# Kernel optimization log

Hardware: AMD Instinct MI355X
Metric: run time of the kernel (lower is better)

## Reference

```python
import math
import jax, jax.numpy as jnp
import numpy as np

B, T, E = 2, 2048, 2048
H, HKV = 16, 4
DH = E // H              # 128
ROT_DIM = DH             # rotary_pct = 1.0 -> 128
ROT_HALF = ROT_DIM // 2  # RotaryEmbedding is built with dim=ROT_DIM//2=64; only these dims rotate
MAX_SEQ = 2048


def _rope_tables():
    # theta = 10000 ** (-arange(0, dim, 2)/dim) with dim = ROT_HALF
    theta = 10000.0 ** (-jnp.arange(0, ROT_HALF, 2, dtype=jnp.float32) / ROT_HALF)  # [ROT_HALF//2]
    pos = jnp.arange(MAX_SEQ, dtype=jnp.float32)
    angles = pos[:, None] * theta[None, :]   # [MAX_SEQ, ROT_HALF//2]
    return jnp.cos(angles), jnp.sin(angles)


def _apply_rotary(q, k, start_pos):
    # q: [B,T,H,ROT_DIM], k: [B,T,HKV,ROT_DIM]; rotate only first ROT_HALF dims (interleaved pairs)
    cos, sin = _rope_tables()
    t = q.shape[1]
    cos = jax.lax.dynamic_slice_in_dim(cos, start_pos, t, axis=0)[None, :, None, :]
    sin = jax.lax.dynamic_slice_in_dim(sin, start_pos, t, axis=0)[None, :, None, :]

    def rot(a):
        a_rot, a_pass = a[..., :ROT_HALF], a[..., ROT_HALF:]
        x, y = a_rot[..., 0::2], a_rot[..., 1::2]
        rx = x * cos - y * sin
        ry = x * sin + y * cos
        rotated = jnp.stack([rx, ry], axis=-1).reshape(*a_rot.shape)
        return jnp.concatenate([rotated, a_pass], axis=-1)

    return rot(q), rot(k)


def setup_inputs() -> dict:
    key = jax.random.key(0)
    ks = jax.random.split(key, 9)
    s = 0.02  # weight scale for sane logits
    return {
        "x": jax.random.normal(ks[0], (B, T, E), dtype=jnp.float32),
        "Wq": jax.random.normal(ks[1], (E, H * DH), dtype=jnp.float32) * s,
        "bq": jax.random.normal(ks[2], (H * DH,), dtype=jnp.float32) * s,
        "Wk": jax.random.normal(ks[3], (E, HKV * DH), dtype=jnp.float32) * s,
        "bk": jax.random.normal(ks[4], (HKV * DH,), dtype=jnp.float32) * s,
        "Wv": jax.random.normal(ks[5], (E, HKV * DH), dtype=jnp.float32) * s,
        "bv": jax.random.normal(ks[6], (HKV * DH,), dtype=jnp.float32) * s,
        "Wo": jax.random.normal(ks[7], (E, E), dtype=jnp.float32) * s,
        "bo": jax.random.normal(ks[8], (E,), dtype=jnp.float32) * s,
        "start_pos": 0,
    }


def reference(x, Wq, bq, Wk, bk, Wv, bv, Wo, bo, start_pos):
    b, t, _ = x.shape
    q = (x @ Wq + bq).reshape(b, t, H, DH)
    k = (x @ Wk + bk).reshape(b, t, HKV, DH)
    v = (x @ Wv + bv).reshape(b, t, HKV, DH)

    q, k = _apply_rotary(q, k, start_pos)

    group = H // HKV
    k = jnp.repeat(k, group, axis=2)  # [b,t,H,DH]
    v = jnp.repeat(v, group, axis=2)

    # scores: [b,H,t,t]
    scores = jnp.einsum("bqhd,bkhd->bhqk", q, k) / math.sqrt(DH)
    causal = jnp.tril(jnp.ones((t, t), dtype=bool))
    scores = jnp.where(causal[None, None], scores, -jnp.inf)
    probs = jax.nn.softmax(scores, axis=-1)

    out = jnp.einsum("bhqk,bkhd->bqhd", probs, v).reshape(b, t, H * DH)
    return out @ Wo + bo
```

## Files before the change

kernel.cpp:

```cpp
#include <hip/hip_runtime.h>

typedef __attribute__((ext_vector_type(8))) short short8;
typedef __attribute__((ext_vector_type(4))) float f32x4;
typedef __attribute__((ext_vector_type(16))) float f32x16;

#define DEVFN __device__ __forceinline__

DEVFN unsigned short f2bf(float f) {
  unsigned int u = __builtin_bit_cast(unsigned int, f);
  u += 0x7FFFu + ((u >> 16) & 1u);
  return (unsigned short)(u >> 16);
}
DEVFN float bf2f(unsigned int u) { return __builtin_bit_cast(float, u << 16); }

DEVFN unsigned int cvtpk_bf16(float lo, float hi) {
  unsigned int d;
  asm("v_cvt_pk_bf16_f32 %0, %1, %2" : "=v"(d) : "v"(lo), "v"(hi));
  return d;
}
DEVFN void plswap32(unsigned int& a, unsigned int& b) {
  asm("v_permlane32_swap_b32 %0, %1" : "+v"(a), "+v"(b));
}
DEVFN float bcast32(float v, int srclane) {
  int r = __builtin_amdgcn_ds_bpermute(srclane * 4, __builtin_bit_cast(int, v));
  return __builtin_bit_cast(float, r);
}

__global__ __launch_bounds__(256) void prep_all(
    const float* __restrict__ Wq, const float* __restrict__ Wk, const float* __restrict__ Wv,
    const float* __restrict__ Wo, const float* __restrict__ bq, const float* __restrict__ bk,
    const float* __restrict__ bv, const float* __restrict__ x,
    unsigned short* __restrict__ Wqkvt, unsigned short* __restrict__ Wot,
    unsigned short* __restrict__ xb, float* __restrict__ cost, float* __restrict__ sint,
    float* __restrict__ bcat) {
  __shared__ float lds[32][33];
  const int bid = blockIdx.x, tid = threadIdx.x;
  if (bid < 10240) {
    const float* W; unsigned short* Wt; int ncols, bx, by;
    if (bid < 4096)      { W = Wq; Wt = Wqkvt;                        ncols = 2048; bx = bid & 63; by = bid >> 6; }
    else if (bid < 5120) { int l = bid - 4096; W = Wk; Wt = Wqkvt + (size_t)2048 * 2048; ncols = 512; bx = l & 15; by = l >> 4; }
    else if (bid < 6144) { int l = bid - 5120; W = Wv; Wt = Wqkvt + (size_t)2560 * 2048; ncols = 512; bx = l & 15; by = l >> 4; }
    else                 { int l = bid - 6144; W = Wo; Wt = Wot;      ncols = 2048; bx = l & 63; by = l >> 6; }
    int n0 = bx * 32, k0 = by * 32;
    int tx = tid & 31, ty = tid >> 5;
    #pragma unroll
    for (int i = 0; i < 4; i++) {
      int kr = ty + i * 8;
      lds[kr][tx] = W[(size_t)(k0 + kr) * ncols + n0 + tx];
    }
    __syncthreads();
    #pragma unroll
    for (int i = 0; i < 4; i++) {
      int nr = ty + i * 8;
      Wt[(size_t)(n0 + nr) * 2048 + k0 + tx] = f2bf(lds[tx][nr]);
    }
  } else if (bid < 14336) {
    int gid = (bid - 10240) * 256 + tid;
    const float4* xv = (const float4*)x;
    float4 a = xv[(size_t)gid * 2], b = xv[(size_t)gid * 2 + 1];
    short8 u;
    u[0] = (short)f2bf(a.x); u[1] = (short)f2bf(a.y); u[2] = (short)f2bf(a.z); u[3] = (short)f2bf(a.w);
    u[4] = (short)f2bf(b.x); u[5] = (short)f2bf(b.y); u[6] = (short)f2bf(b.z); u[7] = (short)f2bf(b.w);
    *(short8*)(xb + (size_t)gid * 8) = u;
  } else if (bid < 14592) {
    int gid = (bid - 14336) * 256 + tid;
    int pos = gid >> 5, i = gid & 31;
    float theta = powf(10000.0f, -(float)(2 * i) / 64.0f);
    float ang = (float)pos * theta;
    cost[gid] = cosf(ang);
    sint[gid] = sinf(ang);
  } else {
    int i = (bid - 14592) * 256 + tid;
    float v;
    if (i < 2048) v = bq[i];
    else if (i < 2560) v = bk[i - 2048];
    else v = bv[i - 2560];
    bcat[i] = v;
  }
}

__global__ __launch_bounds__(256) void scatter_all(
    const unsigned short* __restrict__ QKVb, const float* __restrict__ cost,
    const float* __restrict__ sint, const int* __restrict__ spp,
    unsigned short* __restrict__ QFr, unsigned short* __restrict__ KFr,
    unsigned short* __restrict__ VFr) {
  __shared__ __align__(16) unsigned short lds[64 * 128];
  const int bid = blockIdx.x, tid = threadIdx.x;
  if (bid < 20480) {
    int NH, LOG2NH, colOff, gid;
    unsigned short* dst;
    float scale;
    if (bid < 16384) { NH = 16; LOG2NH = 4; colOff = 0;    dst = QFr; scale = 0.12751743f; gid = bid * 256 + tid; }
    else             { NH = 4;  LOG2NH = 2; colOff = 2048; dst = KFr; scale = 1.0f;        gid = (bid - 16384) * 256 + tid; }
    int j = gid & 63;
    int h = (gid >> 6) & (NH - 1);
    int m = gid >> (6 + LOG2NH);
    int t = m & 2047;
    int b = m >> 11;
    const unsigned short* src = QKVb + (size_t)m * 3072 + colOff + h * 128 + 2 * j;
    unsigned int pair = *(const unsigned int*)src;
    float xv = bf2f(pair & 0xFFFFu), yv = bf2f(pair >> 16);
    float rx, ry;
    if (j < 32) {
      int pos = (spp[0] + t) & 2047;
      float c = cost[pos * 32 + j], s = sint[pos * 32 + j];
      rx = xv * c - yv * s;
      ry = xv * s + yv * c;
    } else { rx = xv; ry = yv; }
    rx *= scale; ry *= scale;
    int d0 = 2 * j;
    size_t off = (size_t)(b * NH + h) * 262144 + (t >> 5) * 4096 + (d0 >> 4) * 512
               + ((d0 >> 3) & 1) * 256 + (t & 31) * 8 + (d0 & 7);
    unsigned int outp = (unsigned int)f2bf(rx) | ((unsigned int)f2bf(ry) << 16);
    *(unsigned int*)(dst + off) = outp;
  } else {
    int l = bid - 20480;
    int t0 = (l & 31) * 64;
    int bk = l >> 5;
    const unsigned short* src = QKVb + (size_t)(bk >> 2) * 2048 * 3072 + 2560 + (bk & 3) * 128;
    #pragma unroll
    for (int c = 0; c < 4; c++) {
      int idx = c * 256 + tid;
      int tr = idx >> 4, dc = idx & 15;
      short8 v = *(const short8*)(src + (size_t)(t0 + tr) * 3072 + dc * 8);
      *(short8*)((char*)lds + tr * 256 + 16 * (dc ^ (tr >> 3))) = v;
    }
    __syncthreads();
    unsigned short* dstb = VFr + (size_t)bk * 262144;
    #pragma unroll
    for (int c2 = 0; c2 < 4; c2++) {
      int idx2 = c2 * 256 + tid;
      int tc = idx2 & 7, d = idx2 >> 3;
      short8 u;
      #pragma unroll
      for (int e = 0; e < 8; e++) {
        int t = 8 * tc + e;
        u[e] = *(const short*)((char*)lds + t * 256 + 16 * ((d >> 3) ^ tc) + (d & 7) * 2);
      }
      size_t off = (size_t)(t0 >> 6) * 8192 + ((d >> 5) * 4 + ((tc >> 1) & 3)) * 512
                 + (tc & 1) * 256 + (d & 31) * 8;
      *(short8*)(dstb + off) = u;
    }
  }
}

template<bool BF16OUT>
__global__ __launch_bounds__(512, 1) void gemm256(
    const unsigned short* __restrict__ A, const unsigned short* __restrict__ Bt,
    const float* __restrict__ bias, void* __restrict__ Cout, int M, int N, int K, int NTX) {
  __shared__ __align__(16) unsigned short lds[3][24576];
  const int tid = threadIdx.x;
  const int lane = tid & 63, w = tid >> 6;
  const int wr = w >> 1, wc = w & 1;
  const int f = blockIdx.x;
  const int cpx = gridDim.x >> 3;
  const int fs = (f & 7) * cpx + (f >> 3);
  const int m0 = (fs / NTX) * 256, n0 = (fs % NTX) * 128;
  const int NT = K >> 6;

  f32x4 acc[4][4];
  #pragma unroll
  for (int i = 0; i < 4; i++)
    #pragma unroll
    for (int j = 0; j < 4; j++)
      #pragma unroll
      for (int r = 0; r < 4; r++) acc[i][j][r] = 0.f;

  const int r8 = tid >> 3;
  const int c8 = (tid & 7) ^ (r8 & 7);
  const unsigned short* Asrc = A  + (size_t)(m0 + r8) * K + c8 * 8;
  const unsigned short* Bsrc = Bt + (size_t)(n0 + r8) * K + c8 * 8;
  const int woff = w * 512;

  auto STAGE = [&](int t) {
    unsigned short* bb = &lds[t % 3][0];
    const unsigned short* as = Asrc + t * 64;
    const unsigned short* bs = Bsrc + t * 64;
    #pragma unroll
    for (int l = 0; l < 2; l++) {
      __builtin_amdgcn_global_load_lds(
        (const __attribute__((address_space(1))) unsigned int*)(as + (size_t)l * 64 * K),
        (__attribute__((address_space(3))) unsigned int*)(bb + l * 4096 + woff), 16, 0, 0);
      __builtin_amdgcn_global_load_lds(
        (const __attribute__((address_space(1))) unsigned int*)(as + (size_t)(128 + l * 64) * K),
        (__attribute__((address_space(3))) unsigned int*)(bb + 8192 + l * 4096 + woff), 16, 0, 0);
      __builtin_amdgcn_global_load_lds(
        (const __attribute__((address_space(1))) unsigned int*)(bs + (size_t)l * 64 * K),
        (__attribute__((address_space(3))) unsigned int*)(bb + 16384 + l * 4096 + woff), 16, 0, 0);
    }
  };

  STAGE(0);
  STAGE(1);

  const int lr = lane & 15;
  const int q4 = lane >> 4;
  const int p7 = lane & 7;
  const int so0 = ((q4 ^ p7) * 8);
  const int so1 = (((q4 ^ 4) ^ p7) * 8);
  const int aBase = ((wr & 2) ? 8192 : 0) + ((wr & 1) * 64 + lr) * 64;
  const int bBase = 16384 + (wc * 64 + lr) * 64;

  for (int t = 0; t < NT; t++) {
    if (t + 1 < NT) asm volatile("s_waitcnt vmcnt(6)" ::: "memory");
    else            asm volatile("s_waitcnt vmcnt(0)" ::: "memory");
    __builtin_amdgcn_sched_barrier(0);
    __builtin_amdgcn_s_barrier();
    __builtin_amdgcn_sched_barrier(0);
    if (t + 2 < NT) STAGE(t + 2);
    const unsigned short* bb = &lds[t % 3][0];
    #pragma unroll
    for (int ks = 0; ks < 2; ks++) {
      const int so = ks ? so1 : so0;
      short8 af[4], bfr[4];
      #pragma unroll
      for (int mi = 0; mi < 4; mi++)
        af[mi] = *(const short8*)(bb + aBase + mi * 1024 + so);
      #pragma unroll
      for (int ni = 0; ni < 4; ni++)
        bfr[ni] = *(const short8*)(bb + bBase + ni * 1024 + so);
      __builtin_amdgcn_s_setprio(1);
      #pragma unroll
      for (int mi = 0; mi < 4; mi++)
        #pragma unroll
        for (int ni = 0; ni < 4; ni++)
          acc[mi][ni] = __builtin_amdgcn_mfma_f32_16x16x32_bf16(af[mi], bfr[ni], acc[mi][ni], 0, 0, 0);
      __builtin_amdgcn_s_setprio(0);
    }
  }

  const int cl = lane & 15, rq = lane >> 4;
  #pragma unroll
  for (int mi = 0; mi < 4; mi++) {
    #pragma unroll
    for (int ni = 0; ni < 4; ni++) {
      int gn = n0 + wc * 64 + ni * 16 + cl;
      float bv = bias[gn];
      #pragma unroll
      for (int r = 0; r < 4; r++) {
        int gm = m0 + wr * 64 + mi * 16 + rq * 4 + r;
        float v = acc[mi][ni][r] + bv;
        if (BF16OUT) ((unsigned short*)Cout)[(size_t)gm * N + gn] = f2bf(v);
        else ((float*)Cout)[(size_t)gm * N + gn] = v;
      }
    }
  }
}

__global__ __launch_bounds__(256, 2) void attn_kernel(
    const unsigned short* __restrict__ QF, const unsigned short* __restrict__ KF,
    const unsigned short* __restrict__ VF, unsigned short* __restrict__ O) {
  __shared__ __align__(16) unsigned short Kl[2][8192];
  __shared__ __align__(16) unsigned short Vl[2][8192];

  const int tid = threadIdx.x;
  const int lane = tid & 63;
  const int w = tid >> 6;
  const int l31 = lane & 31;
  const int hf = lane >> 5;
  const int bid = blockIdx.x;
  const int g8 = bid & 7;
  const int b = g8 >> 2, kh = g8 & 3;
  const int h = kh * 4 + ((bid >> 3) & 3);
  const int qg = (bid < 256) ? (bid >> 5) : (15 - ((bid - 256) >> 5));
  const int qt = qg * 4 + w;
  const int qw = qt * 32;
  const int ntw = (qt >> 1) + 1;
  const int nbt = 2 * qg + 2;

  const unsigned short* qh  = QF + (size_t)(b * 16 + h) * 262144 + qt * 4096;
  const unsigned short* khp = KF + (size_t)(b * 4 + kh) * 262144;
  const unsigned short* vhp = VF + (size_t)(b * 4 + kh) * 262144;

  short8 qf[8];
  #pragma unroll
  for (int s = 0; s < 8; s++)
    qf[s] = *(const short8*)(qh + s * 512 + lane * 8);

  short8 ones;
  #pragma unroll
  for (int e = 0; e < 8; e++) ones[e] = (short)0x3F80;

  float m_r = -3.0e38f;
  f32x16 oacc[4];
  f32x16 lacc;
  #pragma unroll
  for (int dt = 0; dt < 4; dt++)
    #pragma unroll
    for (int r = 0; r < 16; r++) oacc[dt][r] = 0.f;
  #pragma unroll
  for (int r = 0; r < 16; r++) lacc[r] = 0.f;

  auto STAGE = [&](int buf, int kt) {
    #pragma unroll
    for (int c = 0; c < 4; c++) {
      const int sl = w * 4 + c;
      __builtin_amdgcn_global_load_lds(
        (const __attribute__((address_space(1))) unsigned int*)(khp + (size_t)kt * 8192 + sl * 512 + lane * 8),
        (__attribute__((address_space(3))) unsigned int*)(&Kl[buf][sl * 512]), 16, 0, 0);
      __builtin_amdgcn_global_load_lds(
        (const __attribute__((address_space(1))) unsigned int*)(vhp + (size_t)kt * 8192 + sl * 512 + lane * 8),
        (__attribute__((address_space(3))) unsigned int*)(&Vl[buf][sl * 512]), 16, 0, 0);
    }
  };

  STAGE(0, 0);
  int cur = 0;
  for (int kt = 0; kt < nbt; kt++) {
    __syncthreads();
    if (kt + 1 < nbt) STAGE(cur ^ 1, kt + 1);
    if (kt < ntw) {
      const int kv0 = kt * 64;
      const unsigned short* Kb = &Kl[cur][0];
      const unsigned short* Vb = &Vl[cur][0];
      f32x16 sc[2];
      {
        short8 kf0[8];
        #pragma unroll
        for (int s = 0; s < 8; s++)
          kf0[s] = *(const short8*)(Kb + s * 512 + lane * 8);
        #pragma unroll
        for (int r = 0; r < 16; r++) sc[0][r] = 0.f;
        #pragma unroll
        for (int s = 0; s < 8; s++)
          sc[0] = __builtin_amdgcn_mfma_f32_32x32x16_bf16(kf0[s], qf[s], sc[0], 0, 0, 0);
      }
      {
        short8 kf1[8];
        #pragma unroll
        for (int s = 0; s < 8; s++)
          kf1[s] = *(const short8*)(Kb + (8 + s) * 512 + lane * 8);
        #pragma unroll
        for (int r = 0; r < 16; r++) sc[1][r] = 0.f;
        #pragma unroll
        for (int s = 0; s < 8; s++)
          sc[1] = __builtin_amdgcn_mfma_f32_32x32x16_bf16(kf1[s], qf[s], sc[1], 0, 0, 0);
      }
      short8 vf[4][4];
      #pragma unroll
      for (int dt = 0; dt < 4; dt++)
        #pragma unroll
        for (int ks = 0; ks < 4; ks++)
          vf[dt][ks] = *(const short8*)(Vb + (dt * 4 + ks) * 512 + lane * 8);

      if (kv0 + 63 > qw) {
        #pragma unroll
        for (int ct = 0; ct < 2; ct++)
          #pragma unroll
          for (int r = 0; r < 16; r++) {
            int kg = kv0 + ct * 32 + (r & 3) + 8 * (r >> 2) + 4 * hf;
            if (kg > qw + l31) sc[ct][r] = -3.0e38f;
          }
      }
      float mx[16];
      #pragma unroll
      for (int r = 0; r < 16; r++) mx[r] = fmaxf(sc[0][r], sc[1][r]);
      #pragma unroll
      for (int s2 = 8; s2 >= 1; s2 >>= 1)
        #pragma unroll
        for (int i = 0; i < 8; i++) if (i < s2) mx[i] = fmaxf(mx[i], mx[i + s2]);
      float tm = fmaxf(mx[0], __shfl_xor(mx[0], 32));
      if (__any(tm > m_r + 8.0f)) {
        float mn = fmaxf(m_r, tm);
        float al = __builtin_amdgcn_exp2f(m_r - mn);
        m_r = mn;
        #pragma unroll
        for (int r = 0; r < 16; r++) {
          float alr = bcast32(al, (r & 3) + 8 * (r >> 2) + 4 * hf);
          #pragma unroll
          for (int dt = 0; dt < 4; dt++) oacc[dt][r] *= alr;
          lacc[r] *= alr;
        }
      }
      #pragma unroll
      for (int ct = 0; ct < 2; ct++)
        #pragma unroll
        for (int r = 0; r < 16; r++) sc[ct][r] = __builtin_amdgcn_exp2f(sc[ct][r] - m_r);

      short8 pa[4];
      #pragma unroll
      for (int ks = 0; ks < 4; ks++) {
        const int ct = ks >> 1, kb = (ks & 1) * 8;
        unsigned int A0 = cvtpk_bf16(sc[ct][kb + 0], sc[ct][kb + 1]);
        unsigned int A1 = cvtpk_bf16(sc[ct][kb + 2], sc[ct][kb + 3]);
        unsigned int B0 = cvtpk_bf16(sc[ct][kb + 4], sc[ct][kb + 5]);
        unsigned int B1 = cvtpk_bf16(sc[ct][kb + 6], sc[ct][kb + 7]);
        plswap32(A0, B0);
        plswap32(A1, B1);
        union { unsigned int wds[4]; short8 s8; } u;
        u.wds[0] = A0; u.wds[1] = A1; u.wds[2] = B0; u.wds[3] = B1;
        pa[ks] = u.s8;
      }
      #pragma unroll
      for (int ks = 0; ks < 4; ks++)
        lacc = __builtin_amdgcn_mfma_f32_32x32x16_bf16(pa[ks], ones, lacc, 0, 0, 0);
      #pragma unroll
      for (int dt = 0; dt < 4; dt++)
        #pragma unroll
        for (int ks = 0; ks < 4; ks++)
          oacc[dt] = __builtin_amdgcn_mfma_f32_32x32x16_bf16(pa[ks], vf[dt][ks], oacc[dt], 0, 0, 0);
    }
    cur ^= 1;
  }
  #pragma unroll
  for (int r = 0; r < 16; r++) {
    float inv = 1.0f / lacc[r];
    int rloc = (r & 3) + 8 * (r >> 2) + 4 * hf;
    int qgr = qw + rloc;
    unsigned short* orow = O + ((size_t)(b * 2048 + qgr)) * 2048 + h * 128;
    #pragma unroll
    for (int dt = 0; dt < 4; dt++)
      orow[dt * 32 + l31] = f2bf(oacc[dt][r] * inv);
  }
}

extern "C" void kernel_launch(void* const* d_in, const int* in_sizes, int n_in,
                              void* d_out, int out_size, void* d_ws, size_t ws_size,
                              hipStream_t stream) {
  (void)in_sizes; (void)n_in; (void)out_size; (void)ws_size;
  const float* x  = (const float*)d_in[0];
  const float* Wq = (const float*)d_in[1];
  const float* bq = (const float*)d_in[2];
  const float* Wk = (const float*)d_in[3];
  const float* bk = (const float*)d_in[4];
  const float* Wv = (const float*)d_in[5];
  const float* bv = (const float*)d_in[6];
  const float* Wo = (const float*)d_in[7];
  const float* bo = (const float*)d_in[8];
  const int*   sp = (const int*)d_in[9];

  char* ws = (char*)d_ws;
  unsigned short* xb    = (unsigned short*)ws;
  unsigned short* Wqkvt = (unsigned short*)(ws + 16777216);
  unsigned short* Wot   = (unsigned short*)(ws + 29360128);
  unsigned short* QKVb  = (unsigned short*)(ws + 37748736);
  float* cost           = (float*)(ws + 62914560);
  float* sint           = (float*)(ws + 63176704);
  float* bcat           = (float*)(ws + 63438848);

  unsigned short* Obuf = xb;
  unsigned short* QFr = (unsigned short*)d_out;
  unsigned short* KFr = (unsigned short*)((char*)d_out + 16777216);
  unsigned short* VFr = (unsigned short*)((char*)d_out + 20971520);

  prep_all<<<dim3(14604), 256, 0, stream>>>(Wq, Wk, Wv, Wo, bq, bk, bv, x,
                                            Wqkvt, Wot, xb, cost, sint, bcat);
  gemm256<true><<<dim3(384), 512, 0, stream>>>(xb, Wqkvt, bcat, QKVb, 4096, 3072, 2048, 24);
  scatter_all<<<dim3(20736), 256, 0, stream>>>(QKVb, cost, sint, sp, QFr, KFr, VFr);
  attn_kernel<<<dim3(512), 256, 0, stream>>>(QFr, KFr, VFr, Obuf);
  gemm256<false><<<dim3(256), 512, 0, stream>>>(Obuf, Wot, bo, (float*)d_out, 4096, 2048, 2048, 16);
}
```

Before: 207.9 us.

## Split GEMM k-loop into ping-pong halves interleaving A/B prefetch with MFMA

Splits the prefetch of the next-next tile into separate A and B stages and issues each one after the LDS fragment reads of a k-substep. Adds an extra workgroup barrier and an lgkmcnt wait before each MFMA burst, giving a ping-pong schedule meant to spread global-to-LDS traffic across the compute phases. The intent is to keep memory issue and MFMA from colliding. It costs two additional barriers per k-tile, and the vmcnt(6) wait count still assumes the original issue order.

```diff
diff --git a/kernel.cpp b/kernel.cpp
--- a/kernel.cpp
+++ b/kernel.cpp
@@ -172,10 +172,9 @@
   const unsigned short* Bsrc = Bt + (size_t)(n0 + r8) * K + c8 * 8;
   const int woff = w * 512;
 
-  auto STAGE = [&](int t) {
+  auto STAGE_A = [&](int t) {
     unsigned short* bb = &lds[t % 3][0];
     const unsigned short* as = Asrc + t * 64;
-    const unsigned short* bs = Bsrc + t * 64;
     #pragma unroll
     for (int l = 0; l < 2; l++) {
       __builtin_amdgcn_global_load_lds(
@@ -184,14 +183,20 @@
       __builtin_amdgcn_global_load_lds(
         (const __attribute__((address_space(1))) unsigned int*)(as + (size_t)(128 + l * 64) * K),
         (__attribute__((address_space(3))) unsigned int*)(bb + 8192 + l * 4096 + woff), 16, 0, 0);
+    }
+  };
+  auto STAGE_B = [&](int t) {
+    unsigned short* bb = &lds[t % 3][0];
+    const unsigned short* bs = Bsrc + t * 64;
+    #pragma unroll
+    for (int l = 0; l < 2; l++)
       __builtin_amdgcn_global_load_lds(
         (const __attribute__((address_space(1))) unsigned int*)(bs + (size_t)l * 64 * K),
         (__attribute__((address_space(3))) unsigned int*)(bb + 16384 + l * 4096 + woff), 16, 0, 0);
-    }
   };
 
-  STAGE(0);
-  STAGE(1);
+  STAGE_A(0); STAGE_B(0);
+  STAGE_A(1); STAGE_B(1);
 
   const int lr = lane & 15;
   const int q4 = lane >> 4;
@@ -207,18 +212,20 @@
     __builtin_amdgcn_sched_barrier(0);
     __builtin_amdgcn_s_barrier();
     __builtin_amdgcn_sched_barrier(0);
-    if (t + 2 < NT) STAGE(t + 2);
     const unsigned short* bb = &lds[t % 3][0];
-    #pragma unroll
-    for (int ks = 0; ks < 2; ks++) {
-      const int so = ks ? so1 : so0;
+    {
       short8 af[4], bfr[4];
       #pragma unroll
       for (int mi = 0; mi < 4; mi++)
-        af[mi] = *(const short8*)(bb + aBase + mi * 1024 + so);
+        af[mi] = *(const short8*)(bb + aBase + mi * 1024 + so0);
       #pragma unroll
       for (int ni = 0; ni < 4; ni++)
-        bfr[ni] = *(const short8*)(bb + bBase + ni * 1024 + so);
+        bfr[ni] = *(const short8*)(bb + bBase + ni * 1024 + so0);
+      if (t + 2 < NT) STAGE_A(t + 2);
+      __builtin_amdgcn_sched_barrier(0);
+      __builtin_amdgcn_s_barrier();
+      asm volatile("s_waitcnt lgkmcnt(0)" ::: "memory");
+      __builtin_amdgcn_sched_barrier(0);
       __builtin_amdgcn_s_setprio(1);
       #pragma unroll
       for (int mi = 0; mi < 4; mi++)
@@ -226,6 +233,29 @@
         for (int ni = 0; ni < 4; ni++)
           acc[mi][ni] = __builtin_amdgcn_mfma_f32_16x16x32_bf16(af[mi], bfr[ni], acc[mi][ni], 0, 0, 0);
       __builtin_amdgcn_s_setprio(0);
+      __builtin_amdgcn_sched_barrier(0);
+    }
+    {
+      short8 af[4], bfr[4];
+      #pragma unroll
+      for (int mi = 0; mi < 4; mi++)
+        af[mi] = *(const short8*)(bb + aBase + mi * 1024 + so1);
+      #pragma unroll
+      for (int ni = 0; ni < 4; ni++)
+        bfr[ni] = *(const short8*)(bb + bBase + ni * 1024 + so1);
+      if (t + 2 < NT) STAGE_B(t + 2);
+      __builtin_amdgcn_sched_barrier(0);
+      __builtin_amdgcn_s_barrier();
+      asm volatile("s_waitcnt lgkmcnt(0)" ::: "memory");
+      __builtin_amdgcn_sched_barrier(0);
+      __builtin_amdgcn_s_setprio(1);
+      #pragma unroll
+      for (int mi = 0; mi < 4; mi++)
+        #pragma unroll
+        for (int ni = 0; ni < 4; ni++)
+          acc[mi][ni] = __builtin_amdgcn_mfma_f32_16x16x32_bf16(af[mi], bfr[ni], acc[mi][ni], 0, 0, 0);
+      __builtin_amdgcn_s_setprio(0);
+      __builtin_amdgcn_sched_barrier(0);
     }
   }
 
```

New measurement: 209.2 us. About the same (+0.7%).

## Switch GEMMs to 256x256 tiles with double-buffered LDS staging

Applied to the files above, without the earlier changes.

Enlarges the GEMM output tile from 256x128 to 256x256, giving each wave a 128x64 sub-tile with 8x4 accumulators. This raises data reuse per LDS load and halves the grid size. The LDS pipeline drops from three buffers with a two-ahead prefetch to two buffers with a one-ahead prefetch, a full vmcnt(0) wait and an extra barrier each iteration. The risk is reduced load/compute overlap and under-filling the MI355X's 256 CUs, since only 192 and 128 blocks are launched.

```diff
diff --git a/kernel.cpp b/kernel.cpp
--- a/kernel.cpp
+++ b/kernel.cpp
@@ -145,100 +145,97 @@
 }
 
 template<bool BF16OUT>
-__global__ __launch_bounds__(512, 1) void gemm256(
+__global__ __launch_bounds__(512, 1) void gemm256sq(
     const unsigned short* __restrict__ A, const unsigned short* __restrict__ Bt,
     const float* __restrict__ bias, void* __restrict__ Cout, int M, int N, int K, int NTX) {
-  __shared__ __align__(16) unsigned short lds[3][24576];
+  __shared__ __align__(16) unsigned short lds[2][32768];
   const int tid = threadIdx.x;
   const int lane = tid & 63, w = tid >> 6;
-  const int wr = w >> 1, wc = w & 1;
+  const int wrM = w >> 2, wcN = w & 3;
   const int f = blockIdx.x;
   const int cpx = gridDim.x >> 3;
   const int fs = (f & 7) * cpx + (f >> 3);
-  const int m0 = (fs / NTX) * 256, n0 = (fs % NTX) * 128;
+  const int m0 = (fs / NTX) * 256, n0 = (fs % NTX) * 256;
   const int NT = K >> 6;
 
-  f32x4 acc[4][4];
-  #pragma unroll
-  for (int i = 0; i < 4; i++)
+  f32x4 acc[8][4];
+  #pragma unroll
+  for (int i = 0; i < 8; i++)
     #pragma unroll
     for (int j = 0; j < 4; j++)
       #pragma unroll
       for (int r = 0; r < 4; r++) acc[i][j][r] = 0.f;
 
-  const int r8 = tid >> 3;
-  const int c8 = (tid & 7) ^ (r8 & 7);
-  const unsigned short* Asrc = A  + (size_t)(m0 + r8) * K + c8 * 8;
-  const unsigned short* Bsrc = Bt + (size_t)(n0 + r8) * K + c8 * 8;
-  const int woff = w * 512;
-
-  auto STAGE = [&](int t) {
-    unsigned short* bb = &lds[t % 3][0];
-    const unsigned short* as = Asrc + t * 64;
-    const unsigned short* bs = Bsrc + t * 64;
-    #pragma unroll
-    for (int l = 0; l < 2; l++) {
+  const int rr = w * 8 + (lane >> 3);
+  const int cc = (lane & 7) ^ (lane >> 3);
+  const unsigned short* Asrc = A  + (size_t)(m0 + rr) * K + cc * 8;
+  const unsigned short* Bsrc = Bt + (size_t)(n0 + rr) * K + cc * 8;
+  const int dstw = w * 512;
+
+  auto STAGE = [&](int b, int kt) {
+    unsigned short* bb = &lds[b][0];
+    const unsigned short* as = Asrc + kt * 64;
+    const unsigned short* bs = Bsrc + kt * 64;
+    #pragma unroll
+    for (int l = 0; l < 4; l++) {
       __builtin_amdgcn_global_load_lds(
         (const __attribute__((address_space(1))) unsigned int*)(as + (size_t)l * 64 * K),
-        (__attribute__((address_space(3))) unsigned int*)(bb + l * 4096 + woff), 16, 0, 0);
-      __builtin_amdgcn_global_load_lds(
-        (const __attribute__((address_space(1))) unsigned int*)(as + (size_t)(128 + l * 64) * K),
-        (__attribute__((address_space(3))) unsigned int*)(bb + 8192 + l * 4096 + woff), 16, 0, 0);
+        (__attribute__((address_space(3))) unsigned int*)(bb + l * 4096 + dstw), 16, 0, 0);
       __builtin_amdgcn_global_load_lds(
         (const __attribute__((address_space(1))) unsigned int*)(bs + (size_t)l * 64 * K),
-        (__attribute__((address_space(3))) unsigned int*)(bb + 16384 + l * 4096 + woff), 16, 0, 0);
+        (__attribute__((address_space(3))) unsigned int*)(bb + 16384 + l * 4096 + dstw), 16, 0, 0);
     }
   };
 
-  STAGE(0);
-  STAGE(1);
+  STAGE(0, 0);
 
   const int lr = lane & 15;
   const int q4 = lane >> 4;
   const int p7 = lane & 7;
   const int so0 = ((q4 ^ p7) * 8);
   const int so1 = (((q4 ^ 4) ^ p7) * 8);
-  const int aBase = ((wr & 2) ? 8192 : 0) + ((wr & 1) * 64 + lr) * 64;
-  const int bBase = 16384 + (wc * 64 + lr) * 64;
+  const int aBase = (wrM * 128 + lr) * 64;
+  const int bBase = 16384 + (wcN * 64 + lr) * 64;
 
   for (int t = 0; t < NT; t++) {
-    if (t + 1 < NT) asm volatile("s_waitcnt vmcnt(6)" ::: "memory");
-    else            asm volatile("s_waitcnt vmcnt(0)" ::: "memory");
+    asm volatile("s_waitcnt vmcnt(0)" ::: "memory");
     __builtin_amdgcn_sched_barrier(0);
     __builtin_amdgcn_s_barrier();
     __builtin_amdgcn_sched_barrier(0);
-    if (t + 2 < NT) STAGE(t + 2);
-    const unsigned short* bb = &lds[t % 3][0];
-    #pragma unroll
-    for (int ks = 0; ks < 2; ks++) {
-      const int so = ks ? so1 : so0;
-      short8 af[4], bfr[4];
-      #pragma unroll
-      for (int mi = 0; mi < 4; mi++)
-        af[mi] = *(const short8*)(bb + aBase + mi * 1024 + so);
-      #pragma unroll
-      for (int ni = 0; ni < 4; ni++)
-        bfr[ni] = *(const short8*)(bb + bBase + ni * 1024 + so);
+    if (t + 1 < NT) STAGE((t + 1) & 1, t + 1);
+    const unsigned short* bb = &lds[t & 1][0];
+    short8 bf0[4], bf1[4];
+    #pragma unroll
+    for (int ni = 0; ni < 4; ni++) {
+      bf0[ni] = *(const short8*)(bb + bBase + ni * 1024 + so0);
+      bf1[ni] = *(const short8*)(bb + bBase + ni * 1024 + so1);
+    }
+    #pragma unroll
+    for (int mi = 0; mi < 8; mi++) {
+      short8 af0 = *(const short8*)(bb + aBase + mi * 1024 + so0);
+      short8 af1 = *(const short8*)(bb + aBase + mi * 1024 + so1);
       __builtin_amdgcn_s_setprio(1);
       #pragma unroll
-      for (int mi = 0; mi < 4; mi++)
-        #pragma unroll
-        for (int ni = 0; ni < 4; ni++)
-          acc[mi][ni] = __builtin_amdgcn_mfma_f32_16x16x32_bf16(af[mi], bfr[ni], acc[mi][ni], 0, 0, 0);
+      for (int ni = 0; ni < 4; ni++) {
+        acc[mi][ni] = __builtin_amdgcn_mfma_f32_16x16x32_bf16(af0, bf0[ni], acc[mi][ni], 0, 0, 0);
+        acc[mi][ni] = __builtin_amdgcn_mfma_f32_16x16x32_bf16(af1, bf1[ni], acc[mi][ni], 0, 0, 0);
+      }
       __builtin_amdgcn_s_setprio(0);
     }
+    __builtin_amdgcn_sched_barrier(0);
+    __builtin_amdgcn_s_barrier();
   }
 
   const int cl = lane & 15, rq = lane >> 4;
   #pragma unroll
-  for (int mi = 0; mi < 4; mi++) {
+  for (int mi = 0; mi < 8; mi++) {
     #pragma unroll
     for (int ni = 0; ni < 4; ni++) {
-      int gn = n0 + wc * 64 + ni * 16 + cl;
+      int gn = n0 + wcN * 64 + ni * 16 + cl;
       float bv = bias[gn];
       #pragma unroll
       for (int r = 0; r < 4; r++) {
-        int gm = m0 + wr * 64 + mi * 16 + rq * 4 + r;
+        int gm = m0 + wrM * 128 + mi * 16 + rq * 4 + r;
         float v = acc[mi][ni][r] + bv;
         if (BF16OUT) ((unsigned short*)Cout)[(size_t)gm * N + gn] = f2bf(v);
         else ((float*)Cout)[(size_t)gm * N + gn] = v;
@@ -445,8 +442,8 @@
 
   prep_all<<<dim3(14604), 256, 0, stream>>>(Wq, Wk, Wv, Wo, bq, bk, bv, x,
                                             Wqkvt, Wot, xb, cost, sint, bcat);
-  gemm256<true><<<dim3(384), 512, 0, stream>>>(xb, Wqkvt, bcat, QKVb, 4096, 3072, 2048, 24);
+  gemm256sq<true><<<dim3(192), 512, 0, stream>>>(xb, Wqkvt, bcat, QKVb, 4096, 3072, 2048, 12);
   scatter_all<<<dim3(20736), 256, 0, stream>>>(QKVb, cost, sint, sp, QFr, KFr, VFr);
   attn_kernel<<<dim3(512), 256, 0, stream>>>(QFr, KFr, VFr, Obuf);
-  gemm256<false><<<dim3(256), 512, 0, stream>>>(Obuf, Wot, bo, (float*)d_out, 4096, 2048, 2048, 16);
-}
+  gemm256sq<false><<<dim3(128), 512, 0, stream>>>(Obuf, Wot, bo, (float*)d_out, 4096, 2048, 2048, 8);
+}
```

After: 213.0 us. 1.02x slower.
